# Optimization experiments

Hardware: AMD Instinct MI355X
Metric: run time of the kernel (lower is better)

## Reference

```python
import jax, jax.numpy as jnp
import numpy as np

IOU_THRESHOLD = 0.5
NEGATIVE_RATIO = 3
ALPHA = 1.0
B, A, D, G = 64, 8732, 85, 32  # batch, anchors, 4+81 classes, max gt per image


def cxcywh_to_xyxy(b):
    cx, cy, w, h = b[..., 0], b[..., 1], b[..., 2], b[..., 3]
    return jnp.stack([cx - w / 2, cy - h / 2, cx + w / 2, cy + h / 2], axis=-1)


def box_iou(a, b):
    # a: (G,4) xyxy, b: (A,4) xyxy -> (G,A)
    lt = jnp.maximum(a[:, None, :2], b[None, :, :2])
    rb = jnp.minimum(a[:, None, 2:], b[None, :, 2:])
    wh = jnp.clip(rb - lt, 0.0)
    inter = wh[..., 0] * wh[..., 1]
    area_a = (a[:, 2] - a[:, 0]) * (a[:, 3] - a[:, 1])
    area_b = (b[:, 2] - b[:, 0]) * (b[:, 3] - b[:, 1])
    return inter / (area_a[:, None] + area_b[None, :] - inter)


def encode(gt, anchors):
    g_cxcy = (gt[:, :2] - anchors[:, :2]) / anchors[:, 2:]
    g_wh = jnp.log(gt[:, 2:]) - jnp.log(anchors[:, 2:])
    return jnp.concatenate([g_cxcy, g_wh], axis=-1)


def match_one(gt_box, gt_label, count, anchors):
    # gt_box (G,4) cxcywh, gt_label (G,), count scalar, anchors (A,4) cxcywh
    num_anchors = anchors.shape[0]
    valid = jnp.arange(gt_box.shape[0]) < count
    iou = box_iou(cxcywh_to_xyxy(gt_box), cxcywh_to_xyxy(anchors))  # (G,A)
    iou = jnp.where(valid[:, None], iou, -1.0)
    best_gt_overlap = iou.max(0)
    best_gt_idx = iou.argmax(0)
    over = best_gt_overlap > IOU_THRESHOLD
    loc = jnp.where(over[:, None], encode(gt_box[best_gt_idx], anchors), 0.0)
    cls = jnp.where(over, gt_label[best_gt_idx].astype(jnp.float32) + 1.0, 0.0)
    # force-match: each (valid) gt claims its best anchor, overwriting
    best_prior_idx = iou.argmax(1)  # (G,)
    idx = jnp.where(valid, best_prior_idx, num_anchors)  # dump invalid gt into a scratch row
    loc = jnp.concatenate([loc, jnp.zeros((1, 4), loc.dtype)], 0)
    loc = loc.at[idx].set(encode(gt_box, anchors[best_prior_idx]))[:num_anchors]
    cls = jnp.concatenate([cls, jnp.zeros((1,), cls.dtype)], 0)
    cls = cls.at[idx].set(gt_label.astype(jnp.float32) + 1.0)[:num_anchors]
    return loc, cls


def smooth_l1(d):
    ad = jnp.abs(d)
    return jnp.where(ad < 1.0, 0.5 * d * d, ad - 0.5)


def multibox_loss(pred, anchors, gt_boxes, gt_labels, gt_counts):
    num_anchors = pred.shape[1]
    loc_pred, conf_pred = pred[:, :, :4], pred[:, :, 4:]
    target_loc, target_cls = jax.vmap(match_one, in_axes=(0, 0, 0, None))(
        gt_boxes, gt_labels, gt_counts, anchors)  # (B,A,4), (B,A)
    pos = target_cls > 0  # (B,A)
    posf = pos.astype(pred.dtype)
    n_pos = posf.sum(1)  # (B,) guaranteed > 0 since every image has >=1 gt
    # localization: per-element smooth-L1 on positives, normalized per image
    loc_l = smooth_l1(loc_pred - target_loc) * posf[:, :, None]
    loc_loss = jnp.sum(loc_l / n_pos[:, None, None])
    # classification CE per anchor
    logp = jax.nn.log_softmax(conf_pred, axis=-1)  # (B,A,C)
    cls_ce = -jnp.take_along_axis(logp, target_cls.astype(jnp.int32)[:, :, None], axis=-1)[..., 0]
    pos_loss = jnp.sum(cls_ce * posf / n_pos[:, None])
    # hard negative mining (double-sort rank trick, no grad through selection)
    num_neg = jnp.minimum(NEGATIVE_RATIO * pos.sum(1), num_anchors - 1)  # (B,) int
    all_neg = jax.lax.stop_gradient(jnp.where(pos, 0.0, cls_ce))
    order = jnp.argsort(-all_neg, axis=1)
    rank = jnp.argsort(order, axis=1)
    neg_mask = (rank < num_neg[:, None]).astype(pred.dtype)
    neg_ce = -logp[:, :, 0]  # CE against background class 0
    neg_loss = jnp.sum(neg_ce * neg_mask / n_pos[:, None])
    return ALPHA * loc_loss + pos_loss + neg_loss


def setup_inputs() -> dict:
    key = jax.random.key(0)
    k1, k2, k3, k4, k5, k6, k7 = jax.random.split(key, 7)
    pred = jax.random.normal(k1, (B, A, D), dtype=jnp.float32)
    anchors = jnp.concatenate([
        jax.random.uniform(k2, (A, 2), minval=0.0, maxval=1.0),
        jax.random.uniform(k3, (A, 2), minval=0.05, maxval=0.5)], axis=-1)
    gt_boxes = jnp.concatenate([
        jax.random.uniform(k4, (B, G, 2), minval=0.0, maxval=1.0),
        jax.random.uniform(k5, (B, G, 2), minval=0.05, maxval=0.6)], axis=-1)
    gt_labels = jax.random.randint(k6, (B, G), 0, 80)
    gt_counts = jax.random.randint(k7, (B,), 1, G + 1)
    return {"pred": pred, "anchors": anchors, "gt_boxes": gt_boxes,
            "gt_labels": gt_labels, "gt_counts": gt_counts}


def reference(pred, anchors, gt_boxes, gt_labels, gt_counts):
    return multibox_loss(pred, anchors, gt_boxes, gt_labels, gt_counts)
```

## Files before the change

kernel.cpp:

```cpp
#include <hip/hip_runtime.h>
#include <math.h>

#define BB 64
#define AA 8732
#define DD 85
#define GG 32
#define CC 81
#define TILE 64
#define NT 137
#define TPB 12
#define NTB 12
#define NAB 35


typedef __attribute__((address_space(3))) unsigned int lds_u32;
typedef const __attribute__((address_space(1))) unsigned int glb_u32;

__device__ __forceinline__ float smoothl1(float d) {
  float ad = fabsf(d);
  return ad < 1.0f ? 0.5f * d * d : ad - 0.5f;
}

__device__ __forceinline__ float frcp(float x) {
  return __builtin_amdgcn_rcpf(x);
}

__global__ __launch_bounds__(256) void k_match(
    const float* __restrict__ anchors, const float* __restrict__ gt_boxes,
    const int* __restrict__ gt_counts, int* __restrict__ match,
    int* __restrict__ bestp, int* __restrict__ n_pos)
{
  const int b = blockIdx.y;
  const int count = gt_counts[b];
  __shared__ float gx0[GG], gy0[GG], gx1[GG], gy1[GG], gar[GG];
  __shared__ float wv[4];
  __shared__ int wi[4];

  if (blockIdx.x < NAB) {
    if (blockIdx.x == 0 && threadIdx.x == 0) n_pos[b] = 0;
    if (threadIdx.x < GG) {
      float4 gb = reinterpret_cast<const float4*>(gt_boxes)[b * GG + threadIdx.x];
      float x0 = gb.x - gb.z * 0.5f, y0 = gb.y - gb.w * 0.5f;
      float x1 = gb.x + gb.z * 0.5f, y1 = gb.y + gb.w * 0.5f;
      gx0[threadIdx.x] = x0; gy0[threadIdx.x] = y0;
      gx1[threadIdx.x] = x1; gy1[threadIdx.x] = y1;
      gar[threadIdx.x] = (x1 - x0) * (y1 - y0);
    }
    __syncthreads();
    const int a = blockIdx.x * 256 + threadIdx.x;
    if (a >= AA) return;

    float4 an = reinterpret_cast<const float4*>(anchors)[a];
    float ax0 = an.x - an.z * 0.5f, ay0 = an.y - an.w * 0.5f;
    float ax1 = an.x + an.z * 0.5f, ay1 = an.y + an.w * 0.5f;
    float aar = (ax1 - ax0) * (ay1 - ay0);
    float best = -1.0f; int bi = 0;
    for (int g = 0; g < count; ++g) {
      float iw = fmaxf(fminf(gx1[g], ax1) - fmaxf(gx0[g], ax0), 0.0f);
      float ih = fmaxf(fminf(gy1[g], ay1) - fmaxf(gy0[g], ay0), 0.0f);
      float inter = iw * ih;
      float iou = inter * frcp(gar[g] + aar - inter);
      if (iou > best) { best = iou; bi = g; }
    }
    match[b * AA + a] = (best > 0.5f) ? bi : -1;
  } else {
    const int g = blockIdx.x - NAB;
    if (g >= count) return;

    float4 gb = reinterpret_cast<const float4*>(gt_boxes)[b * GG + g];
    const float gx0s = gb.x - gb.z * 0.5f, gy0s = gb.y - gb.w * 0.5f;
    const float gx1s = gb.x + gb.z * 0.5f, gy1s = gb.y + gb.w * 0.5f;
    const float gars = (gx1s - gx0s) * (gy1s - gy0s);

    float bv = -2.0f; int bi = AA;
    for (int a = threadIdx.x; a < AA; a += 256) {
      float4 an = reinterpret_cast<const float4*>(anchors)[a];
      float ax0 = an.x - an.z * 0.5f, ay0 = an.y - an.w * 0.5f;
      float ax1 = an.x + an.z * 0.5f, ay1 = an.y + an.w * 0.5f;
      float aar = (ax1 - ax0) * (ay1 - ay0);
      float iw = fmaxf(fminf(gx1s, ax1) - fmaxf(gx0s, ax0), 0.0f);
      float ih = fmaxf(fminf(gy1s, ay1) - fmaxf(gy0s, ay0), 0.0f);
      float inter = iw * ih;
      float iou = inter * frcp(gars + aar - inter);
      if (iou > bv || (iou == bv && a < bi)) { bv = iou; bi = a; }
    }
    #pragma unroll
    for (int m = 1; m < 64; m <<= 1) {
      float ov = __shfl_xor(bv, m);
      int   oi = __shfl_xor(bi, m);
      if (ov > bv || (ov == bv && oi < bi)) { bv = ov; bi = oi; }
    }
    if ((threadIdx.x & 63) == 0) { wv[threadIdx.x >> 6] = bv; wi[threadIdx.x >> 6] = bi; }
    __syncthreads();
    if (threadIdx.x == 0) {
      float fv = wv[0]; int fi = wi[0];
      #pragma unroll
      for (int w = 1; w < 4; ++w)
        if (wv[w] > fv || (wv[w] == fv && wi[w] < fi)) { fv = wv[w]; fi = wi[w]; }
      bestp[b * GG + g] = fi;
    }
  }
}

__global__ __launch_bounds__(64) void k_scatter(
    const int* __restrict__ gt_counts, const int* __restrict__ bestp,
    int* __restrict__ match)
{
  const int b = blockIdx.x;
  if (threadIdx.x == 0) {
    const int count = gt_counts[b];
    for (int g = 0; g < count; ++g) match[b * AA + bestp[b * GG + g]] = g;
  }
}

__global__ __launch_bounds__(256) void k_loss(
    const float* __restrict__ pred, const float* __restrict__ anchors,
    const float* __restrict__ gt_boxes, const int* __restrict__ gt_labels,
    const int* __restrict__ match, float* __restrict__ all_neg,
    float* __restrict__ partials, int* __restrict__ n_pos)
{
  const int b = blockIdx.y;
  const int t0 = blockIdx.x * TPB;
  const int t1 = min(t0 + TPB, NT);
  __shared__ float bufs[2][TILE * DD];
  __shared__ int slab[GG];
  __shared__ float wsum[4];
  __shared__ int wcnt[4];

  if (threadIdx.x < GG) slab[threadIdx.x] = gt_labels[b * GG + threadIdx.x];

  #define PREFETCH(t, bufp)                                                  \
    do {                                                                     \
      const int a0_ = (t) * TILE;                                            \
      const int nch_ = (min(TILE, AA - a0_) * DD) >> 2;                      \
      const float* s_ = pred + ((size_t)b * AA + a0_) * DD;                  \
      _Pragma("unroll")                                                      \
      for (int j_ = 0; j_ < 6; ++j_) {                                       \
        int c_ = j_ * 256 + (int)threadIdx.x;                                \
        if (c_ < nch_)                                                       \
          __builtin_amdgcn_global_load_lds(                                  \
              (glb_u32*)(s_ + c_ * 4), (lds_u32*)((bufp) + c_ * 4), 16, 0, 0);\
      }                                                                      \
    } while (0)

  PREFETCH(t0, &bufs[0][0]);
  __syncthreads();

  const int r = threadIdx.x >> 2;
  const int sub = threadIdx.x & 3;
  float acc = 0.0f;
  int poscnt = 0;
  int cur = 0;

  for (int t = t0; t < t1; ++t) {
    if (t + 1 < t1) {
      PREFETCH(t + 1, &bufs[cur ^ 1][0]);
      __builtin_amdgcn_sched_barrier(0);
    }

    const int a0 = t * TILE;
    const int nr = min(TILE, AA - a0);
    const float* rows = &bufs[cur][0];

    if (r < nr) {
      const int a = a0 + r;
      const int m = match[b * AA + a];

      const float* row = rows + r * DD + 4;
      float v[21];
      float mx = -INFINITY;
      #pragma unroll
      for (int k = 0; k < 21; ++k) {
        const int cc = 4 * k + sub;
        float x = (cc < CC) ? row[cc] : -INFINITY;
        v[k] = x;
        mx = fmaxf(mx, x);
      }
      #pragma unroll
      for (int msk = 1; msk <= 2; msk <<= 1)
        mx = fmaxf(mx, __shfl_xor(mx, msk));
      float s = 0.0f;
      #pragma unroll
      for (int k = 0; k < 21; ++k) s += __expf(v[k] - mx);
      #pragma unroll
      for (int msk = 1; msk <= 2; msk <<= 1) s += __shfl_xor(s, msk);
      const float lse = mx + __logf(s);

      if (sub == 0) {
        if (m >= 0) {
          poscnt += 1;
          const int tgt = slab[m] + 1;
          float cls_ce = lse - row[tgt];
          float4 an = reinterpret_cast<const float4*>(anchors)[a];
          float4 gb = reinterpret_cast<const float4*>(gt_boxes)[b * GG + m];
          float tx = (gb.x - an.x) / an.z;
          float ty = (gb.y - an.y) / an.w;
          float tw = __logf(gb.z) - __logf(an.z);
          float th = __logf(gb.w) - __logf(an.w);
          acc += smoothl1(rows[r * DD + 0] - tx)
               + smoothl1(rows[r * DD + 1] - ty)
               + smoothl1(rows[r * DD + 2] - tw)
               + smoothl1(rows[r * DD + 3] - th)
               + cls_ce;
          all_neg[b * AA + a] = 0.0f;
        } else {
          float ce = lse - row[0];
          all_neg[b * AA + a] = fmaxf(ce, 0.0f);
        }
      }
    }

    __syncthreads();
    cur ^= 1;
  }

  #pragma unroll
  for (int msk = 1; msk < 64; msk <<= 1) {
    acc    += __shfl_xor(acc, msk);
    poscnt += __shfl_xor(poscnt, msk);
  }
  if ((threadIdx.x & 63) == 0) {
    wsum[threadIdx.x >> 6] = acc;
    wcnt[threadIdx.x >> 6] = poscnt;
  }
  __syncthreads();
  if (threadIdx.x == 0) {
    partials[b * NTB + blockIdx.x] = (wsum[0] + wsum[1]) + (wsum[2] + wsum[3]);
    int c = wcnt[0] + wcnt[1] + wcnt[2] + wcnt[3];
    if (c) atomicAdd(&n_pos[b], c);
  }
  #undef PREFETCH
}

__global__ __launch_bounds__(1024) void k_select(
    const float* __restrict__ all_neg, const float* __restrict__ partials,
    const int* __restrict__ n_pos, float* __restrict__ batch_total)
{
  const int b = blockIdx.x;
  __shared__ unsigned u[AA];
  __shared__ int hist16[16][257];
  __shared__ int hist[256];
  __shared__ int gsum[64];
  __shared__ unsigned sh_pref;
  __shared__ int sh_k;
  __shared__ float wf[16];
  __shared__ int wc[16];

  {
    const float* srcg = all_neg + (size_t)b * AA;
    #pragma unroll
    for (int j = 0; j < 3; ++j) {
      int c = j * 1024 + threadIdx.x;
      if (c < 2183) {
        __builtin_amdgcn_global_load_lds(
            (glb_u32*)(srcg + c * 4), (lds_u32*)((float*)u + c * 4), 16, 0, 0);
      }
    }
  }
  __syncthreads();

  const int np = n_pos[b];
  const int K = min(3 * np, AA - 1);
  const int wvid = threadIdx.x >> 6;

  unsigned prefix = 0;
  int kk = K;
  for (int shift = 24; shift >= 0; shift -= 8) {
    int* hflat = &hist16[0][0];
    for (int i = threadIdx.x; i < 16 * 257; i += 1024) hflat[i] = 0;
    __syncthreads();
    const unsigned hmask = (shift == 24) ? 0u : (0xFFFFFFFFu << (shift + 8));
    for (int i = threadIdx.x; i < AA; i += 1024) {
      unsigned x = u[i];
      if ((x & hmask) == prefix)
        atomicAdd(&hist16[wvid][(x >> shift) & 255], 1);
    }
    __syncthreads();
    if (threadIdx.x < 256) {
      int s = 0;
      #pragma unroll
      for (int h = 0; h < 16; ++h) s += hist16[h][threadIdx.x];
      hist[threadIdx.x] = s;
    }
    __syncthreads();
    if (threadIdx.x < 64) {
      int base = 255 - 4 * threadIdx.x;
      gsum[threadIdx.x] = hist[base] + hist[base - 1] + hist[base - 2] + hist[base - 3];
    }
    __syncthreads();
    if (threadIdx.x == 0) {
      int cum = 0, chosen = 0;
      const int kv = kk;
      for (int t = 0; t < 64; ++t) {
        int gs = gsum[t];
        if (cum + gs < kv) { cum += gs; continue; }
        for (int bin = 255 - 4 * t; bin >= 252 - 4 * t; --bin) {
          int h = hist[bin];
          if (cum + h >= kv) { chosen = bin; break; }
          cum += h;
        }
        break;
      }
      sh_pref = prefix | ((unsigned)chosen << shift);
      sh_k = kk - cum;
    }
    __syncthreads();
    prefix = sh_pref;
    kk = sh_k;
    __syncthreads();
  }
  const float tstar = __uint_as_float(prefix);

  float ssum = 0.0f; int cgt = 0;
  for (int i = threadIdx.x; i < AA; i += 1024) {
    float x = __uint_as_float(u[i]);
    if (x > tstar) { ssum += x; cgt += 1; }
  }
  #pragma unroll
  for (int m = 1; m < 64; m <<= 1) {
    ssum += __shfl_xor(ssum, m);
    cgt  += __shfl_xor(cgt, m);
  }
  if ((threadIdx.x & 63) == 0) { wf[wvid] = ssum; wc[wvid] = cgt; }
  __syncthreads();
  if (threadIdx.x == 0) {
    float S = 0.0f; int Cg = 0;
    for (int w = 0; w < 16; ++w) { S += wf[w]; Cg += wc[w]; }
    float neg_sum = S + (float)(K - Cg) * tstar;
    float ps = 0.0f;
    for (int t = 0; t < NTB; ++t) ps += partials[b * NTB + t];
    batch_total[b] = (ps + neg_sum) / (float)np;
  }
}

__global__ __launch_bounds__(64) void k_final(
    const float* __restrict__ batch_total, float* __restrict__ out)
{
  float v = batch_total[threadIdx.x];
  #pragma unroll
  for (int m = 1; m < 64; m <<= 1) v += __shfl_xor(v, m);
  if (threadIdx.x == 0) out[0] = v;
}

extern "C" void kernel_launch(void* const* d_in, const int* in_sizes, int n_in,
                              void* d_out, int out_size, void* d_ws, size_t ws_size,
                              hipStream_t stream) {
  (void)in_sizes; (void)n_in; (void)out_size; (void)ws_size;
  const float* pred      = (const float*)d_in[0];
  const float* anchors   = (const float*)d_in[1];
  const float* gt_boxes  = (const float*)d_in[2];
  const int*   gt_labels = (const int*)d_in[3];
  const int*   gt_counts = (const int*)d_in[4];

  char* ws = (char*)d_ws;
  int*   match       = (int*)(ws + 0);
  int*   n_pos       = (int*)(ws + 2235392);
  float* all_neg     = (float*)(ws + 2235648);
  float* partials    = (float*)(ws + 4471040);
  float* batch_total = (float*)(ws + 4506112);
  int*   bestp       = (int*)(ws + 4506368);
  float* out = (float*)d_out;

  hipLaunchKernelGGL(k_match, dim3(NAB + GG, BB), dim3(256), 0, stream,
                     anchors, gt_boxes, gt_counts, match, bestp, n_pos);
  hipLaunchKernelGGL(k_scatter, dim3(BB), dim3(64), 0, stream,
                     gt_counts, bestp, match);
  hipLaunchKernelGGL(k_loss, dim3(NTB, BB), dim3(256), 0, stream,
                     pred, anchors, gt_boxes, gt_labels, match,
                     all_neg, partials, n_pos);
  hipLaunchKernelGGL(k_select, dim3(BB), dim3(1024), 0, stream,
                     all_neg, partials, n_pos, batch_total);
  hipLaunchKernelGGL(k_final, dim3(1), dim3(64), 0, stream, batch_total, out);
}
```

Before: 97.05 us.

## Fuse scatter, select and final reduction into match and loss kernels

Removes the separate scatter, selection and final-sum kernels. The force-match overrides are now applied inside the loss kernel through a per-block shared-memory override table built from bestp. The last loss block finishing for each batch, detected with an atomic counter, runs the radix top-k negative selection using only 256 threads and reused LDS. The last batch to finish then writes the global sum. This cuts three launches and their gaps, in exchange for serialising the selection onto a single 256-thread block per batch at the tail and adding threadfence/atomic completion logic.

After: 131.3 us. 35.2% more time.

```diff
diff --git a/kernel.cpp b/kernel.cpp
--- a/kernel.cpp
+++ b/kernel.cpp
@@ -11,6 +11,7 @@
 #define TPB 12
 #define NTB 12
 #define NAB 35
+#define BLKANCH (TPB * TILE)
 
 
 typedef __attribute__((address_space(3))) unsigned int lds_u32;
@@ -28,7 +29,8 @@
 __global__ __launch_bounds__(256) void k_match(
     const float* __restrict__ anchors, const float* __restrict__ gt_boxes,
     const int* __restrict__ gt_counts, int* __restrict__ match,
-    int* __restrict__ bestp, int* __restrict__ n_pos)
+    int* __restrict__ bestp, int* __restrict__ n_pos,
+    int* __restrict__ done_l, int* __restrict__ done_sel)
 {
   const int b = blockIdx.y;
   const int count = gt_counts[b];
@@ -37,7 +39,11 @@
   __shared__ int wi[4];
 
   if (blockIdx.x < NAB) {
-    if (blockIdx.x == 0 && threadIdx.x == 0) n_pos[b] = 0;
+    if (blockIdx.x == 0 && threadIdx.x == 0) {
+      n_pos[b] = 0;
+      done_l[b] = 0;
+      if (b == 0) *done_sel = 0;
+    }
     if (threadIdx.x < GG) {
       float4 gb = reinterpret_cast<const float4*>(gt_boxes)[b * GG + threadIdx.x];
       float x0 = gb.x - gb.z * 0.5f, y0 = gb.y - gb.w * 0.5f;
@@ -48,86 +54,85 @@
     }
     __syncthreads();
     const int a = blockIdx.x * 256 + threadIdx.x;
-    if (a >= AA) return;
-
-    float4 an = reinterpret_cast<const float4*>(anchors)[a];
-    float ax0 = an.x - an.z * 0.5f, ay0 = an.y - an.w * 0.5f;
-    float ax1 = an.x + an.z * 0.5f, ay1 = an.y + an.w * 0.5f;
-    float aar = (ax1 - ax0) * (ay1 - ay0);
-    float best = -1.0f; int bi = 0;
-    for (int g = 0; g < count; ++g) {
-      float iw = fmaxf(fminf(gx1[g], ax1) - fmaxf(gx0[g], ax0), 0.0f);
-      float ih = fmaxf(fminf(gy1[g], ay1) - fmaxf(gy0[g], ay0), 0.0f);
-      float inter = iw * ih;
-      float iou = inter * frcp(gar[g] + aar - inter);
-      if (iou > best) { best = iou; bi = g; }
-    }
-    match[b * AA + a] = (best > 0.5f) ? bi : -1;
-  } else {
-    const int g = blockIdx.x - NAB;
-    if (g >= count) return;
-
-    float4 gb = reinterpret_cast<const float4*>(gt_boxes)[b * GG + g];
-    const float gx0s = gb.x - gb.z * 0.5f, gy0s = gb.y - gb.w * 0.5f;
-    const float gx1s = gb.x + gb.z * 0.5f, gy1s = gb.y + gb.w * 0.5f;
-    const float gars = (gx1s - gx0s) * (gy1s - gy0s);
-
-    float bv = -2.0f; int bi = AA;
-    for (int a = threadIdx.x; a < AA; a += 256) {
+    if (a < AA) {
       float4 an = reinterpret_cast<const float4*>(anchors)[a];
       float ax0 = an.x - an.z * 0.5f, ay0 = an.y - an.w * 0.5f;
       float ax1 = an.x + an.z * 0.5f, ay1 = an.y + an.w * 0.5f;
       float aar = (ax1 - ax0) * (ay1 - ay0);
-      float iw = fmaxf(fminf(gx1s, ax1) - fmaxf(gx0s, ax0), 0.0f);
-      float ih = fmaxf(fminf(gy1s, ay1) - fmaxf(gy0s, ay0), 0.0f);
-      float inter = iw * ih;
-      float iou = inter * frcp(gars + aar - inter);
-      if (iou > bv || (iou == bv && a < bi)) { bv = iou; bi = a; }
-    }
-    #pragma unroll
-    for (int m = 1; m < 64; m <<= 1) {
-      float ov = __shfl_xor(bv, m);
-      int   oi = __shfl_xor(bi, m);
-      if (ov > bv || (ov == bv && oi < bi)) { bv = ov; bi = oi; }
-    }
-    if ((threadIdx.x & 63) == 0) { wv[threadIdx.x >> 6] = bv; wi[threadIdx.x >> 6] = bi; }
-    __syncthreads();
-    if (threadIdx.x == 0) {
-      float fv = wv[0]; int fi = wi[0];
-      #pragma unroll
-      for (int w = 1; w < 4; ++w)
-        if (wv[w] > fv || (wv[w] == fv && wi[w] < fi)) { fv = wv[w]; fi = wi[w]; }
-      bestp[b * GG + g] = fi;
-    }
-  }
-}
-
-__global__ __launch_bounds__(64) void k_scatter(
-    const int* __restrict__ gt_counts, const int* __restrict__ bestp,
-    int* __restrict__ match)
-{
-  const int b = blockIdx.x;
-  if (threadIdx.x == 0) {
-    const int count = gt_counts[b];
-    for (int g = 0; g < count; ++g) match[b * AA + bestp[b * GG + g]] = g;
+      float best = -1.0f; int bi = 0;
+      for (int g = 0; g < count; ++g) {
+        float iw = fmaxf(fminf(gx1[g], ax1) - fmaxf(gx0[g], ax0), 0.0f);
+        float ih = fmaxf(fminf(gy1[g], ay1) - fmaxf(gy0[g], ay0), 0.0f);
+        float inter = iw * ih;
+        float iou = inter * frcp(gar[g] + aar - inter);
+        if (iou > best) { best = iou; bi = g; }
+      }
+      match[b * AA + a] = (best > 0.5f) ? bi : -1;
+    }
+  } else {
+    const int g = blockIdx.x - NAB;
+    if (g < count) {
+      float4 gb = reinterpret_cast<const float4*>(gt_boxes)[b * GG + g];
+      const float gx0s = gb.x - gb.z * 0.5f, gy0s = gb.y - gb.w * 0.5f;
+      const float gx1s = gb.x + gb.z * 0.5f, gy1s = gb.y + gb.w * 0.5f;
+      const float gars = (gx1s - gx0s) * (gy1s - gy0s);
+
+      float bv = -2.0f; int bi = AA;
+      for (int a = threadIdx.x; a < AA; a += 256) {
+        float4 an = reinterpret_cast<const float4*>(anchors)[a];
+        float ax0 = an.x - an.z * 0.5f, ay0 = an.y - an.w * 0.5f;
+        float ax1 = an.x + an.z * 0.5f, ay1 = an.y + an.w * 0.5f;
+        float aar = (ax1 - ax0) * (ay1 - ay0);
+        float iw = fmaxf(fminf(gx1s, ax1) - fmaxf(gx0s, ax0), 0.0f);
+        float ih = fmaxf(fminf(gy1s, ay1) - fmaxf(gy0s, ay0), 0.0f);
+        float inter = iw * ih;
+        float iou = inter * frcp(gars + aar - inter);
+        if (iou > bv || (iou == bv && a < bi)) { bv = iou; bi = a; }
+      }
+      #pragma unroll
+      for (int m = 1; m < 64; m <<= 1) {
+        float ov = __shfl_xor(bv, m);
+        int   oi = __shfl_xor(bi, m);
+        if (ov > bv || (ov == bv && oi < bi)) { bv = ov; bi = oi; }
+      }
+      if ((threadIdx.x & 63) == 0) { wv[threadIdx.x >> 6] = bv; wi[threadIdx.x >> 6] = bi; }
+      __syncthreads();
+      if (threadIdx.x == 0) {
+        float fv = wv[0]; int fi = wi[0];
+        #pragma unroll
+        for (int w = 1; w < 4; ++w)
+          if (wv[w] > fv || (wv[w] == fv && wi[w] < fi)) { fv = wv[w]; fi = wi[w]; }
+        bestp[b * GG + g] = fi;
+      }
+    }
   }
 }
 
 __global__ __launch_bounds__(256) void k_loss(
     const float* __restrict__ pred, const float* __restrict__ anchors,
     const float* __restrict__ gt_boxes, const int* __restrict__ gt_labels,
-    const int* __restrict__ match, float* __restrict__ all_neg,
-    float* __restrict__ partials, int* __restrict__ n_pos)
+    const int* __restrict__ gt_counts, const int* __restrict__ match,
+    const int* __restrict__ bestp, float* __restrict__ all_neg,
+    float* __restrict__ partials, int* __restrict__ n_pos,
+    int* __restrict__ done_l, int* __restrict__ done_sel,
+    float* __restrict__ batch_total, float* __restrict__ out)
 {
   const int b = blockIdx.y;
   const int t0 = blockIdx.x * TPB;
   const int t1 = min(t0 + TPB, NT);
+  const int abase = t0 * TILE;
+  const int tid = threadIdx.x;
   __shared__ float bufs[2][TILE * DD];
+  __shared__ int ovrblk[BLKANCH];
   __shared__ int slab[GG];
   __shared__ float wsum[4];
   __shared__ int wcnt[4];
-
-  if (threadIdx.x < GG) slab[threadIdx.x] = gt_labels[b * GG + threadIdx.x];
+  __shared__ int sflag;
+  __shared__ unsigned sh_pref;
+  __shared__ int sh_k;
+
+  if (tid < GG) slab[tid] = gt_labels[b * GG + tid];
+  for (int i = tid; i < BLKANCH; i += 256) ovrblk[i] = -1;
 
   #define PREFETCH(t, bufp)                                                  \
     do {                                                                     \
@@ -136,7 +141,7 @@
       const float* s_ = pred + ((size_t)b * AA + a0_) * DD;                  \
       _Pragma("unroll")                                                      \
       for (int j_ = 0; j_ < 6; ++j_) {                                       \
-        int c_ = j_ * 256 + (int)threadIdx.x;                                \
+        int c_ = j_ * 256 + tid;                                             \
         if (c_ < nch_)                                                       \
           __builtin_amdgcn_global_load_lds(                                  \
               (glb_u32*)(s_ + c_ * 4), (lds_u32*)((bufp) + c_ * 4), 16, 0, 0);\
@@ -146,8 +151,14 @@
   PREFETCH(t0, &bufs[0][0]);
   __syncthreads();
 
-  const int r = threadIdx.x >> 2;
-  const int sub = threadIdx.x & 3;
+  if (tid < GG && tid < gt_counts[b]) {
+    int p = bestp[b * GG + tid];
+    if (p >= abase && p < abase + BLKANCH) atomicMax(&ovrblk[p - abase], tid);
+  }
+  __syncthreads();
+
+  const int r = tid >> 2;
+  const int sub = tid & 3;
   float acc = 0.0f;
   int poscnt = 0;
   int cur = 0;
@@ -164,7 +175,8 @@
 
     if (r < nr) {
       const int a = a0 + r;
-      const int m = match[b * AA + a];
+      int m = match[b * AA + a];
+      { int o = ovrblk[a - abase]; if (o >= 0) m = o; }
 
       const float* row = rows + r * DD + 4;
       float v[21];
@@ -219,127 +231,118 @@
     acc    += __shfl_xor(acc, msk);
     poscnt += __shfl_xor(poscnt, msk);
   }
-  if ((threadIdx.x & 63) == 0) {
-    wsum[threadIdx.x >> 6] = acc;
-    wcnt[threadIdx.x >> 6] = poscnt;
+  if ((tid & 63) == 0) {
+    wsum[tid >> 6] = acc;
+    wcnt[tid >> 6] = poscnt;
   }
   __syncthreads();
-  if (threadIdx.x == 0) {
+  if (tid == 0) {
     partials[b * NTB + blockIdx.x] = (wsum[0] + wsum[1]) + (wsum[2] + wsum[3]);
     int c = wcnt[0] + wcnt[1] + wcnt[2] + wcnt[3];
     if (c) atomicAdd(&n_pos[b], c);
-  }
-  #undef PREFETCH
-}
-
-__global__ __launch_bounds__(1024) void k_select(
-    const float* __restrict__ all_neg, const float* __restrict__ partials,
-    const int* __restrict__ n_pos, float* __restrict__ batch_total)
-{
-  const int b = blockIdx.x;
-  __shared__ unsigned u[AA];
-  __shared__ int hist16[16][257];
-  __shared__ int hist[256];
-  __shared__ int gsum[64];
-  __shared__ unsigned sh_pref;
-  __shared__ int sh_k;
-  __shared__ float wf[16];
-  __shared__ int wc[16];
-
-  {
+    __threadfence();
+    int old = atomicAdd(&done_l[b], 1);
+    sflag = (old == NTB - 1) ? 1 : 0;
+  }
+  __syncthreads();
+
+  if (sflag) {
+    __threadfence();
+    char* sbase = (char*)&bufs[0][0];
+    unsigned* u = (unsigned*)sbase;
+    int* hist4  = (int*)(sbase + 34944);
+    int* hist   = (int*)(sbase + 39056);
+    int* gsum   = (int*)(sbase + 40080);
+
     const float* srcg = all_neg + (size_t)b * AA;
     #pragma unroll
-    for (int j = 0; j < 3; ++j) {
-      int c = j * 1024 + threadIdx.x;
-      if (c < 2183) {
+    for (int j = 0; j < 9; ++j) {
+      int c = j * 256 + tid;
+      if (c < 2183)
         __builtin_amdgcn_global_load_lds(
             (glb_u32*)(srcg + c * 4), (lds_u32*)((float*)u + c * 4), 16, 0, 0);
-      }
-    }
-  }
-  __syncthreads();
-
-  const int np = n_pos[b];
-  const int K = min(3 * np, AA - 1);
-  const int wvid = threadIdx.x >> 6;
-
-  unsigned prefix = 0;
-  int kk = K;
-  for (int shift = 24; shift >= 0; shift -= 8) {
-    int* hflat = &hist16[0][0];
-    for (int i = threadIdx.x; i < 16 * 257; i += 1024) hflat[i] = 0;
+    }
     __syncthreads();
-    const unsigned hmask = (shift == 24) ? 0u : (0xFFFFFFFFu << (shift + 8));
-    for (int i = threadIdx.x; i < AA; i += 1024) {
-      unsigned x = u[i];
-      if ((x & hmask) == prefix)
-        atomicAdd(&hist16[wvid][(x >> shift) & 255], 1);
-    }
+
+    const int np = n_pos[b];
+    const int K = min(3 * np, AA - 1);
+    const int wvid = tid >> 6;
+
+    unsigned prefix = 0;
+    int kk = K;
+    for (int shift = 24; shift >= 0; shift -= 8) {
+      for (int i = tid; i < 4 * 257; i += 256) hist4[i] = 0;
+      __syncthreads();
+      const unsigned hmask = (shift == 24) ? 0u : (0xFFFFFFFFu << (shift + 8));
+      for (int i = tid; i < AA; i += 256) {
+        unsigned x = u[i];
+        if ((x & hmask) == prefix)
+          atomicAdd(&hist4[wvid * 257 + ((x >> shift) & 255)], 1);
+      }
+      __syncthreads();
+      {
+        int s = hist4[tid] + hist4[257 + tid] + hist4[514 + tid] + hist4[771 + tid];
+        hist[tid] = s;
+      }
+      __syncthreads();
+      if (tid < 64) {
+        int base = 255 - 4 * tid;
+        gsum[tid] = hist[base] + hist[base - 1] + hist[base - 2] + hist[base - 3];
+      }
+      __syncthreads();
+      if (tid == 0) {
+        int cum = 0, chosen = 0;
+        const int kv = kk;
+        for (int t = 0; t < 64; ++t) {
+          int gs = gsum[t];
+          if (cum + gs < kv) { cum += gs; continue; }
+          for (int bin = 255 - 4 * t; bin >= 252 - 4 * t; --bin) {
+            int h = hist[bin];
+            if (cum + h >= kv) { chosen = bin; break; }
+            cum += h;
+          }
+          break;
+        }
+        sh_pref = prefix | ((unsigned)chosen << shift);
+        sh_k = kk - cum;
+      }
+      __syncthreads();
+      prefix = sh_pref;
+      kk = sh_k;
+      __syncthreads();
+    }
+    const float tstar = __uint_as_float(prefix);
+
+    float ssum = 0.0f; int cgt = 0;
+    for (int i = tid; i < AA; i += 256) {
+      float x = __uint_as_float(u[i]);
+      if (x > tstar) { ssum += x; cgt += 1; }
+    }
+    #pragma unroll
+    for (int m = 1; m < 64; m <<= 1) {
+      ssum += __shfl_xor(ssum, m);
+      cgt  += __shfl_xor(cgt, m);
+    }
+    if ((tid & 63) == 0) { wsum[wvid] = ssum; wcnt[wvid] = cgt; }
     __syncthreads();
-    if (threadIdx.x < 256) {
-      int s = 0;
-      #pragma unroll
-      for (int h = 0; h < 16; ++h) s += hist16[h][threadIdx.x];
-      hist[threadIdx.x] = s;
-    }
-    __syncthreads();
-    if (threadIdx.x < 64) {
-      int base = 255 - 4 * threadIdx.x;
-      gsum[threadIdx.x] = hist[base] + hist[base - 1] + hist[base - 2] + hist[base - 3];
-    }
-    __syncthreads();
-    if (threadIdx.x == 0) {
-      int cum = 0, chosen = 0;
-      const int kv = kk;
-      for (int t = 0; t < 64; ++t) {
-        int gs = gsum[t];
-        if (cum + gs < kv) { cum += gs; continue; }
-        for (int bin = 255 - 4 * t; bin >= 252 - 4 * t; --bin) {
-          int h = hist[bin];
-          if (cum + h >= kv) { chosen = bin; break; }
-          cum += h;
-        }
-        break;
-      }
-      sh_pref = prefix | ((unsigned)chosen << shift);
-      sh_k = kk - cum;
-    }
-    __syncthreads();
-    prefix = sh_pref;
-    kk = sh_k;
-    __syncthreads();
-  }
-  const float tstar = __uint_as_float(prefix);
-
-  float ssum = 0.0f; int cgt = 0;
-  for (int i = threadIdx.x; i < AA; i += 1024) {
-    float x = __uint_as_float(u[i]);
-    if (x > tstar) { ssum += x; cgt += 1; }
-  }
-  #pragma unroll
-  for (int m = 1; m < 64; m <<= 1) {
-    ssum += __shfl_xor(ssum, m);
-    cgt  += __shfl_xor(cgt, m);
-  }
-  if ((threadIdx.x & 63) == 0) { wf[wvid] = ssum; wc[wvid] = cgt; }
-  __syncthreads();
-  if (threadIdx.x == 0) {
-    float S = 0.0f; int Cg = 0;
-    for (int w = 0; w < 16; ++w) { S += wf[w]; Cg += wc[w]; }
-    float neg_sum = S + (float)(K - Cg) * tstar;
-    float ps = 0.0f;
-    for (int t = 0; t < NTB; ++t) ps += partials[b * NTB + t];
-    batch_total[b] = (ps + neg_sum) / (float)np;
-  }
-}
-
-__global__ __launch_bounds__(64) void k_final(
-    const float* __restrict__ batch_total, float* __restrict__ out)
-{
-  float v = batch_total[threadIdx.x];
-  #pragma unroll
-  for (int m = 1; m < 64; m <<= 1) v += __shfl_xor(v, m);
-  if (threadIdx.x == 0) out[0] = v;
+    if (tid == 0) {
+      float S = (wsum[0] + wsum[1]) + (wsum[2] + wsum[3]);
+      int Cg = wcnt[0] + wcnt[1] + wcnt[2] + wcnt[3];
+      float neg_sum = S + (float)(K - Cg) * tstar;
+      float ps = 0.0f;
+      for (int t = 0; t < NTB; ++t) ps += partials[b * NTB + t];
+      batch_total[b] = (ps + neg_sum) / (float)np;
+      __threadfence();
+      int old = atomicAdd(done_sel, 1);
+      if (old == BB - 1) {
+        __threadfence();
+        float s = 0.0f;
+        for (int bb = 0; bb < BB; ++bb) s += batch_total[bb];
+        out[0] = s;
+      }
+    }
+  }
+  #undef PREFETCH
 }
 
 extern "C" void kernel_launch(void* const* d_in, const int* in_sizes, int n_in,
@@ -354,21 +357,20 @@
 
   char* ws = (char*)d_ws;
   int*   match       = (int*)(ws + 0);
-  int*   n_pos       = (int*)(ws + 2235392);
-  float* all_neg     = (float*)(ws + 2235648);
-  float* partials    = (float*)(ws + 4471040);
-  float* batch_total = (float*)(ws + 4506112);
-  int*   bestp       = (int*)(ws + 4506368);
+  float* all_neg     = (float*)(ws + 2235392);
+  float* partials    = (float*)(ws + 4470784);
+  float* batch_total = (float*)(ws + 4473856);
+  int*   bestp       = (int*)(ws + 4474112);
+  int*   n_pos       = (int*)(ws + 4482304);
+  int*   done_l      = (int*)(ws + 4482560);
+  int*   done_sel    = (int*)(ws + 4482816);
   float* out = (float*)d_out;
 
   hipLaunchKernelGGL(k_match, dim3(NAB + GG, BB), dim3(256), 0, stream,
-                     anchors, gt_boxes, gt_counts, match, bestp, n_pos);
-  hipLaunchKernelGGL(k_scatter, dim3(BB), dim3(64), 0, stream,
-                     gt_counts, bestp, match);
+                     anchors, gt_boxes, gt_counts, match, bestp,
+                     n_pos, done_l, done_sel);
   hipLaunchKernelGGL(k_loss, dim3(NTB, BB), dim3(256), 0, stream,
-                     pred, anchors, gt_boxes, gt_labels, match,
-                     all_neg, partials, n_pos);
-  hipLaunchKernelGGL(k_select, dim3(BB), dim3(1024), 0, stream,
-                     all_neg, partials, n_pos, batch_total);
-  hipLaunchKernelGGL(k_final, dim3(1), dim3(64), 0, stream, batch_total, out);
-}
+                     pred, anchors, gt_boxes, gt_labels, gt_counts, match, bestp,
+                     all_neg, partials, n_pos, done_l, done_sel,
+                     batch_total, out);
+}
```
